# Performance work log

Measured on AMD Instinct MI355X. Metric: run time of the kernel, lower is better.

Reference implementation:

```python
import jax, jax.numpy as jnp
import numpy as np

N = 32768
F0, F1, F2, F3 = 16, 32, 64, 128
D0, D1, D2, D3 = (128, 128, 128), (64, 64, 64), (32, 32, 32), (16, 16, 16)
DST1, DST2, DTF = (16, 16, 16, 64), (64, 64, 32, 16), (4, 4, 4, 65536)
FST1, FST2, FTF = 64, 8, 8
TOTAL = 7 * (F0 + F1 + F2 + F3) + 9 * FST1 + 9 * FST2 + FTF  # 2336
INNER = 64
FACE3 = np.array([[1,0,0],[-1,0,0],[0,1,0],[0,-1,0],[0,0,1],[0,0,-1]], np.int32)
ST8 = np.concatenate([np.concatenate([FACE3, np.zeros((6,1), np.int32)], 1),
                      np.array([[0,0,0,1],[0,0,0,-1]], np.int32)], 0)

def rmsnorm(x, scale, eps=1e-8):
    rms = jnp.sqrt(jnp.mean(x * x, axis=-1, keepdims=True))
    return scale * x / (rms + eps)

def geglu(x):
    a, g = jnp.split(x, 2, axis=-1)
    return a * jax.nn.gelu(g)

def table_feats(table, p, offsets):
    # p in [0,1)^D -> scaled integer indices; gather base + modulo-wrapped neighbors
    dims = np.array(table.shape[:-1], np.int32)
    idx = (p * (dims - 1)).astype(jnp.int32)  # [N, D]
    base = table[tuple(idx[:, i] for i in range(idx.shape[-1]))]  # [N, F]
    if offsets is None:
        return base
    nbr = (idx[:, None, :] + offsets[None]) % dims  # [N, K, D]
    nf = table[tuple(nbr[..., i] for i in range(nbr.shape[-1]))]  # [N, K, F]
    return jnp.concatenate([base, nf.reshape(nf.shape[0], -1)], axis=-1)

def setup_inputs():
    key = jax.random.key(0)
    ks = jax.random.split(key, 20)
    tbl = lambda k, dims, f: jax.random.normal(k, dims + (f,), jnp.float32) * 0.1
    lin = lambda k, i, o: jax.random.normal(k, (i, o), jnp.float32) / np.sqrt(i).astype(np.float32)
    return dict(
        pos=jax.random.normal(ks[0], (N, 3), jnp.float32),
        dir=jax.random.normal(ks[1], (N, 3), jnp.float32),
        t=jax.random.uniform(ks[2], (N,), jnp.float32),
        table0=tbl(ks[3], D0, F0), table1=tbl(ks[4], D1, F1),
        table2=tbl(ks[5], D2, F2), table3=tbl(ks[6], D3, F3),
        st1=tbl(ks[7], DST1, FST1), st2=tbl(ks[8], DST2, FST2), tf=tbl(ks[9], DTF, FTF),
        sph_proj=lin(ks[10], 3, 8), tb1=jnp.zeros((1,), jnp.float32), tb2=jnp.zeros((1,), jnp.float32),
        gn1=jnp.ones((12,), jnp.float32), gw1=lin(ks[11], 12, 32),
        gn2=jnp.ones((16,), jnp.float32), gw2=lin(ks[12], 16, 32),
        gn3=jnp.ones((16,), jnp.float32), gw3=lin(ks[13], 16, 3),
        vn1=jnp.ones((TOTAL,), jnp.float32), vw1=lin(ks[14], TOTAL, 2 * TOTAL),
        vn2=jnp.ones((TOTAL,), jnp.float32), vw2=lin(ks[15], TOTAL, INNER),
        fw=lin(ks[16], INNER + 4, 4), fb=jnp.zeros((4,), jnp.float32))

def _forward(pos, dir, t, table0, table1, table2, table3, st1, st2, tf,
             sph_proj, tb1, tb2, gn1, gw1, gn2, gw2, gn3, gw3,
             vn1, vw1, vn2, vw2, fw, fb):
    # SphericalEmbedding
    rho = jnp.sqrt(jnp.sum(pos * pos, axis=-1, keepdims=True))
    phi = jnp.arctan2(pos[:, 1], pos[:, 0])
    theta = jnp.arccos(jnp.clip(pos[:, 2] / rho[:, 0], -1.0, 1.0))
    sph = jnp.stack([rho[:, 0], phi, theta], axis=-1) @ sph_proj  # [N, 8]
    # TimeEmbedding
    ct = jnp.cos(t[:, None] + tb1)
    st_ = jnp.sin(t[:, None] + tb2)
    temb = jnp.concatenate([ct, st_, jax.nn.silu(ct), jax.nn.silu(st_)], axis=-1)  # [N, 4]
    # geometric projection MLP -> normalized lookup coords
    h = jnp.concatenate([sph, temb], axis=-1)  # [N, 12]
    h = geglu(rmsnorm(h, gn1) @ gw1)  # [N, 16]
    h = geglu(rmsnorm(h, gn2) @ gw2)  # [N, 16]
    p = jax.nn.sigmoid(rmsnorm(h, gn3) @ gw3)  # [N, 3] in (0,1)
    pt = jnp.concatenate([p, t[:, None]], axis=-1)  # [N, 4]
    # multi-resolution gathers: base + 6 face neighbors per spatial table
    allf = jnp.concatenate([
        table_feats(table0, p, FACE3), table_feats(table1, p, FACE3),
        table_feats(table2, p, FACE3), table_feats(table3, p, FACE3),
        table_feats(st1, pt, ST8), table_feats(st2, pt, ST8),
        table_feats(tf, pt, None)], axis=-1)  # [N, TOTAL]
    # value MLP
    v = geglu(rmsnorm(allf, vn1) @ vw1)  # [N, TOTAL]
    down = rmsnorm(v, vn2) @ vw2  # [N, INNER]
    final_in = jnp.concatenate([down, p, t[:, None]], axis=-1)  # [N, INNER+4]
    return final_in @ fw + fb  # [N, 4]

def reference(pos, dir, t, table0, table1, table2, table3, st1, st2, tf,
              sph_proj, tb1, tb2, gn1, gw1, gn2, gw2, gn3, gw3,
              vn1, vw1, vn2, vw2, fw, fb):
    return _forward(pos, dir, t, table0, table1, table2, table3, st1, st2, tf,
                    sph_proj, tb1, tb2, gn1, gw1, gn2, gw2, gn3, gw3,
                    vn1, vw1, vn2, vw2, fw, fb)
```

## Files before the change

kernel.cpp:

```cpp
#include <hip/hip_runtime.h>
#include <hip/hip_bf16.h>
#include <stdint.h>

typedef __hip_bfloat16 bf16;
typedef __attribute__((ext_vector_type(8))) short v8s;
typedef __attribute__((ext_vector_type(4))) float v4f;

#define NPTS 32768
#define KTOT 2336
#define MPH2 2432
#define NBX2 19

#define AS1C(p) ((const __attribute__((address_space(1))) void*)(p))
#define AS3(p)  ((__attribute__((address_space(3))) void*)(p))

__device__ __forceinline__ float sigm(float x){ return 1.0f/(1.0f + expf(-x)); }
__device__ __forceinline__ float gelu_tanh(float x){
  float u = 0.7978845608028654f*(x + 0.044715f*x*x*x);
  return 0.5f*x*(1.0f + tanhf(u));
}
__device__ __forceinline__ float gelu_fast(float x){
  float u = 1.5957691216057308f*x*(1.0f + 0.044715f*x*x);
  return x / (1.0f + __expf(-u));
}

__global__ __launch_bounds__(256) void k_preamble(
    const float* __restrict__ pos, const float* __restrict__ t,
    const float* __restrict__ sph_proj, const float* __restrict__ tb1,
    const float* __restrict__ tb2,
    const float* __restrict__ gn1, const float* __restrict__ gw1,
    const float* __restrict__ gn2, const float* __restrict__ gw2,
    const float* __restrict__ gn3, const float* __restrict__ gw3,
    float4* __restrict__ Pbuf)
{
  int i = blockIdx.x*256 + threadIdx.x;
  if(i >= NPTS) return;
  float px = pos[3*i], py = pos[3*i+1], pz = pos[3*i+2];
  float rho = sqrtf(px*px + py*py + pz*pz);
  float phi = atan2f(py, px);
  float cz = fminf(1.0f, fmaxf(-1.0f, pz/rho));
  float theta = acosf(cz);
  float tv = t[i];
  float h[12];
  #pragma unroll
  for(int j=0;j<8;j++)
    h[j] = rho*sph_proj[j] + phi*sph_proj[8+j] + theta*sph_proj[16+j];
  float ct = cosf(tv + tb1[0]);
  float st = sinf(tv + tb2[0]);
  h[8]=ct; h[9]=st; h[10]=ct*sigm(ct); h[11]=st*sigm(st);

  float ss = 0.f;
  #pragma unroll
  for(int j=0;j<12;j++) ss += h[j]*h[j];
  float den = sqrtf(ss/12.0f) + 1e-8f;
  float hn[12];
  #pragma unroll
  for(int j=0;j<12;j++) hn[j] = gn1[j]*h[j]/den;

  float h2[16];
  #pragma unroll
  for(int j=0;j<16;j++){
    float a=0.f, g=0.f;
    #pragma unroll
    for(int k=0;k<12;k++){ a += hn[k]*gw1[k*32+j]; g += hn[k]*gw1[k*32+16+j]; }
    h2[j] = a*gelu_tanh(g);
  }
  ss = 0.f;
  #pragma unroll
  for(int j=0;j<16;j++) ss += h2[j]*h2[j];
  den = sqrtf(ss/16.0f) + 1e-8f;
  float hn2[16];
  #pragma unroll
  for(int j=0;j<16;j++) hn2[j] = gn2[j]*h2[j]/den;

  float h3[16];
  #pragma unroll
  for(int j=0;j<16;j++){
    float a=0.f, g=0.f;
    #pragma unroll
    for(int k=0;k<16;k++){ a += hn2[k]*gw2[k*32+j]; g += hn2[k]*gw2[k*32+16+j]; }
    h3[j] = a*gelu_tanh(g);
  }
  ss = 0.f;
  #pragma unroll
  for(int j=0;j<16;j++) ss += h3[j]*h3[j];
  den = sqrtf(ss/16.0f) + 1e-8f;
  float q[3];
  #pragma unroll
  for(int j=0;j<3;j++){
    float a=0.f;
    #pragma unroll
    for(int k=0;k<16;k++) a += (gn3[k]*h3[k]/den)*gw3[k*3+j];
    q[j] = sigm(a);
  }
  Pbuf[i] = make_float4(q[0], q[1], q[2], tv);
}

template<int F, int R>
__device__ __forceinline__ float rows_copyT(const float* __restrict__ T,
    const int (&offs)[R], bf16* __restrict__ dst, int lane){
  float ss = 0.f;
  if constexpr (F >= 64){
    #pragma unroll
    for(int r=0;r<R;r++){
      #pragma unroll
      for(int f0=0; f0<F; f0+=64){
        float v = T[(size_t)offs[r] + f0 + lane];
        dst[r*F + f0 + lane] = __float2bfloat16(v);
        ss += v*v;
      }
    }
  } else {
    constexpr int RPP = 64/F;
    int sub = lane / F;
    int f   = lane & (F-1);
    #pragma unroll
    for(int r0=0;r0<R;r0+=RPP){
      int r = r0 + sub;
      if(r < R){
        float v = T[(size_t)offs[r] + f];
        dst[r*F + f] = __float2bfloat16(v);
        ss += v*v;
      }
    }
  }
  return ss;
}

template<int F>
__device__ __forceinline__ float table3_gather(const float* __restrict__ T, int d,
    float p0, float p1, float p2, bf16* __restrict__ dst, int lane){
  int ix = (int)(p0*(float)(d-1));
  int iy = (int)(p1*(float)(d-1));
  int iz = (int)(p2*(float)(d-1));
  int xp = (ix+1>=d)?0:ix+1, xm = (ix==0)?d-1:ix-1;
  int yp = (iy+1>=d)?0:iy+1, ym = (iy==0)?d-1:iy-1;
  int zp = (iz+1>=d)?0:iz+1, zm = (iz==0)?d-1:iz-1;
  int offs[7] = {
    ((ix*d+iy)*d+iz)*F, ((xp*d+iy)*d+iz)*F, ((xm*d+iy)*d+iz)*F,
    ((ix*d+yp)*d+iz)*F, ((ix*d+ym)*d+iz)*F,
    ((ix*d+iy)*d+zp)*F, ((ix*d+iy)*d+zm)*F };
  return rows_copyT<F,7>(T, offs, dst, lane);
}

template<int F>
__device__ __forceinline__ float table4_gather(const float* __restrict__ T,
    int d0,int d1,int d2,int d3,
    float p0,float p1,float p2,float p3, bf16* __restrict__ dst, int lane){
  int ix = (int)(p0*(float)(d0-1));
  int iy = (int)(p1*(float)(d1-1));
  int iz = (int)(p2*(float)(d2-1));
  int iw = (int)(p3*(float)(d3-1));
  int xp=(ix+1>=d0)?0:ix+1, xm=(ix==0)?d0-1:ix-1;
  int yp=(iy+1>=d1)?0:iy+1, ym=(iy==0)?d1-1:iy-1;
  int zp=(iz+1>=d2)?0:iz+1, zm=(iz==0)?d2-1:iz-1;
  int wp=(iw+1>=d3)?0:iw+1, wm=(iw==0)?d3-1:iw-1;
  #define RO(x,y,z,w) (((((x)*d1 + (y))*d2 + (z))*d3 + (w))*F)
  int offs[9] = {
    RO(ix,iy,iz,iw), RO(xp,iy,iz,iw), RO(xm,iy,iz,iw),
    RO(ix,yp,iz,iw), RO(ix,ym,iz,iw), RO(ix,iy,zp,iw), RO(ix,iy,zm,iw),
    RO(ix,iy,iz,wp), RO(ix,iy,iz,wm) };
  #undef RO
  return rows_copyT<F,9>(T, offs, dst, lane);
}

__global__ __launch_bounds__(256) void k_gather(
    const float4* __restrict__ Pbuf,
    const float* __restrict__ T0, const float* __restrict__ T1,
    const float* __restrict__ T2, const float* __restrict__ T3,
    const float* __restrict__ S1, const float* __restrict__ S2,
    const float* __restrict__ TF,
    bf16* __restrict__ X, float* __restrict__ sx)
{
  int wave = threadIdx.x>>6, lane = threadIdx.x&63;
  int ptid = blockIdx.x*4 + wave;
  float4 P = Pbuf[ptid];
  bf16* dst = X + (size_t)ptid*KTOT;
  float ss = 0.f;
  ss += table3_gather<16 >(T0, 128, P.x, P.y, P.z, dst + 0,    lane);
  ss += table3_gather<32 >(T1,  64, P.x, P.y, P.z, dst + 112,  lane);
  ss += table3_gather<64 >(T2,  32, P.x, P.y, P.z, dst + 336,  lane);
  ss += table3_gather<128>(T3,  16, P.x, P.y, P.z, dst + 784,  lane);
  ss += table4_gather<64>(S1, 16,16,16,64, P.x,P.y,P.z,P.w, dst + 1680, lane);
  ss += table4_gather<8 >(S2, 64,64,32,16, P.x,P.y,P.z,P.w, dst + 2256, lane);
  {
    int ix=(int)(P.x*3.0f), iy=(int)(P.y*3.0f), iz=(int)(P.z*3.0f);
    int iw=(int)(P.w*65535.0f);
    int offs[1] = { (int)((((ix*4+iy)*4+iz))*65536 + iw)*8 };
    ss += rows_copyT<8,1>(TF, offs, dst + 2328, lane);
  }
  #pragma unroll
  for(int o=32;o>0;o>>=1) ss += __shfl_xor(ss, o);
  if(lane==0) sx[ptid] = 1.0f/(sqrtf(ss/2336.0f) + 1e-8f);
}

#define W1B_U4 ((2*MPH2*KTOT*2)/16)
__global__ __launch_bounds__(256) void k_w1zero(uint4* __restrict__ W1b){
  size_t idx = (size_t)blockIdx.x*256 + threadIdx.x;
  if(idx < (size_t)W1B_U4)
    W1b[idx] = make_uint4(0u,0u,0u,0u);
}

__global__ __launch_bounds__(256) void k_w1prep(const float* __restrict__ vw1,
                                                const float* __restrict__ vn1,
                                                bf16* __restrict__ W1b)
{
  __shared__ float tile[32][33];
  int h  = blockIdx.z;
  int m0 = blockIdx.x*32, k0 = blockIdx.y*32;
  int tx = threadIdx.x & 31, ty = threadIdx.x >> 5;
  #pragma unroll
  for(int dy=0; dy<32; dy+=8){
    int k = k0 + ty + dy;
    tile[ty+dy][tx] = vw1[(size_t)k*4672 + h*2336 + m0 + tx] * vn1[k];
  }
  __syncthreads();
  #pragma unroll
  for(int dy=0; dy<32; dy+=8){
    int m = m0 + ty + dy;
    W1b[(size_t)(h*MPH2 + m)*KTOT + k0 + tx] = __float2bfloat16(tile[tx][ty+dy]);
  }
}

__global__ __launch_bounds__(256) void k_w2prep(const float* __restrict__ vw2,
                                                const float* __restrict__ vn2,
                                                const float* __restrict__ fw,
                                                float4* __restrict__ W2f)
{
  int k = blockIdx.x*256 + threadIdx.x;
  if(k >= KTOT) return;
  float a0=0,a1=0,a2=0,a3=0;
  for(int i=0;i<64;i++){
    float w = vw2[k*64+i];
    a0 += w*fw[i*4+0]; a1 += w*fw[i*4+1]; a2 += w*fw[i*4+2]; a3 += w*fw[i*4+3];
  }
  float s = vn2[k];
  W2f[k] = make_float4(s*a0, s*a1, s*a2, s*a3);
}


#define PIPE_WAIT(NSTR) do{                                   \
    __builtin_amdgcn_sched_barrier(0);                        \
    asm volatile("s_waitcnt vmcnt(" NSTR ")" ::: "memory");   \
    __builtin_amdgcn_s_barrier();                             \
  }while(0)

template<int SB>
__device__ __forceinline__ void stage4(const bf16* aSrc, const bf16* bSrc, int k0e,
    bf16 (&As)[4][8192], bf16 (&Bs)[4][8192], int wave)
{
  __builtin_amdgcn_global_load_lds(AS1C(aSrc + k0e),            AS3(&As[SB][wave*512]),        16, 0, 0);
  __builtin_amdgcn_global_load_lds(AS1C(aSrc + 128*KTOT + k0e), AS3(&As[SB][4096 + wave*512]), 16, 0, 0);
  __builtin_amdgcn_global_load_lds(AS1C(bSrc + k0e),            AS3(&Bs[SB][wave*512]),        16, 0, 0);
  __builtin_amdgcn_global_load_lds(AS1C(bSrc + 64*KTOT + k0e),  AS3(&Bs[SB][4096 + wave*512]), 16, 0, 0);
}

template<int RB, int SB, bool STG>
__device__ __forceinline__ void body(const bf16* aSrc, const bf16* bSrc, int k0e,
    bf16 (&As)[4][8192], bf16 (&Bs)[4][8192], int wave, int aOff, int bOff,
    v4f (&acc)[8][4])
{
  v8s af[8]; v8s bb[4];
  #pragma unroll
  for(int i=0;i<8;i++) af[i] = *(const v8s*)(&As[RB][aOff + i*512]);
  #pragma unroll
  for(int j=0;j<4;j++) bb[j] = *(const v8s*)(&Bs[RB][bOff + j*512]);
  if constexpr (STG) stage4<SB>(aSrc, bSrc, k0e, As, Bs, wave);
  #pragma unroll
  for(int i=0;i<8;i++)
    #pragma unroll
    for(int j=0;j<4;j++)
      acc[i][j] = __builtin_amdgcn_mfma_f32_16x16x32_bf16(af[i], bb[j], acc[i][j], 0,0,0);
}

__global__ __launch_bounds__(512, 2) void k_gemm1(
    const bf16* __restrict__ X, const bf16* __restrict__ W1b,
    const float* __restrict__ sx, const float4* __restrict__ W2f,
    float* __restrict__ Part)
{
  __shared__ bf16 As[4][8192];
  __shared__ bf16 Bs[4][8192];
  int tid = threadIdx.x;
  int wave = tid>>6, lane = tid&63;

  int lid = blockIdx.x + 19*blockIdx.y;
  int swz = (lid & 7)*304 + (lid >> 3);
  int bx = swz % 19;
  int by = swz / 19;
  int row0 = by*256;
  int colh = bx*128;

  int wm = wave>>2, wn = wave&3;
  int lm = lane&15, lq = lane>>4;

  v4f acc[8][4];
  #pragma unroll
  for(int i=0;i<8;i++)
    #pragma unroll
    for(int j=0;j<4;j++)
      acc[i][j] = (v4f){0.f,0.f,0.f,0.f};

  int r0 = tid>>2;
  int qa = (tid&3) ^ ((tid>>3)&3);
  const bf16* aSrc = X + (size_t)(row0 + r0)*KTOT + qa*8;
  const bf16* bSrc = W1b + (size_t)(((r0>>5)&1)*MPH2 + colh + (r0>>6)*32 + (r0&31))*KTOT + qa*8;

  int swz4 = lq ^ ((lm>>1)&3);
  int aOff = ((wm*128 + lm)*4 + swz4)*8;
  int bOff = ((wn*64  + lm)*4 + swz4)*8;

  stage4<0>(aSrc, bSrc, 0,  As, Bs, wave);
  stage4<1>(aSrc, bSrc, 32, As, Bs, wave);
  stage4<2>(aSrc, bSrc, 64, As, Bs, wave);
  PIPE_WAIT("8");

  for(int t=0; t<68; t+=4){
    int ke = (t+3)*32;
    body<0,3,true>(aSrc,bSrc,ke,    As,Bs,wave,aOff,bOff,acc); PIPE_WAIT("8");
    body<1,0,true>(aSrc,bSrc,ke+32, As,Bs,wave,aOff,bOff,acc); PIPE_WAIT("8");
    body<2,1,true>(aSrc,bSrc,ke+64, As,Bs,wave,aOff,bOff,acc); PIPE_WAIT("8");
    body<3,2,true>(aSrc,bSrc,ke+96, As,Bs,wave,aOff,bOff,acc); PIPE_WAIT("8");
  }
  body<0,3,true >(aSrc,bSrc,71*32, As,Bs,wave,aOff,bOff,acc); PIPE_WAIT("8");
  body<1,0,true >(aSrc,bSrc,72*32, As,Bs,wave,aOff,bOff,acc); PIPE_WAIT("8");
  body<2,0,false>(aSrc,bSrc,0,     As,Bs,wave,aOff,bOff,acc); PIPE_WAIT("4");
  body<3,0,false>(aSrc,bSrc,0,     As,Bs,wave,aOff,bOff,acc); PIPE_WAIT("0");
  body<0,0,false>(aSrc,bSrc,0,     As,Bs,wave,aOff,bOff,acc);
  __syncthreads();

  float* red = (float*)&As[0][0];
  #pragma unroll
  for(int ph=0; ph<4; ph++){
    if(wn == ph){
      #pragma unroll
      for(int i=0;i<8;i++){
        #pragma unroll
        for(int r=0;r<4;r++){
          int lrow = wm*128 + i*16 + lq*4 + r;
          float s = sx[row0 + lrow];
          float d0=0,d1=0,d2=0,d3=0,ssq=0;
          #pragma unroll
          for(int j=0;j<2;j++){
            int c = colh + wn*32 + j*16 + lm;
            float va = s*acc[i][j][r];
            float vg = s*acc[i][j+2][r];
            float v  = va * gelu_fast(vg);
            int ci = c < KTOT ? c : KTOT-1;
            float4 w = W2f[ci];
            d0 += v*w.x; d1 += v*w.y; d2 += v*w.z; d3 += v*w.w;
            ssq += v*v;
          }
          #pragma unroll
          for(int o=1;o<16;o<<=1){
            d0 += __shfl_xor(d0,o); d1 += __shfl_xor(d1,o);
            d2 += __shfl_xor(d2,o); d3 += __shfl_xor(d3,o);
            ssq += __shfl_xor(ssq,o);
          }
          if(lm==0){
            if(ph==0){
              red[lrow*8+0]=d0; red[lrow*8+1]=d1; red[lrow*8+2]=d2;
              red[lrow*8+3]=d3; red[lrow*8+4]=ssq;
              red[lrow*8+5]=0.f; red[lrow*8+6]=0.f; red[lrow*8+7]=0.f;
            } else {
              red[lrow*8+0]+=d0; red[lrow*8+1]+=d1; red[lrow*8+2]+=d2;
              red[lrow*8+3]+=d3; red[lrow*8+4]+=ssq;
            }
          }
        }
      }
    }
    __syncthreads();
  }
  {
    int rr = tid >> 1, c4 = (tid & 1)*4;
    float4 val = *(float4*)&red[rr*8 + c4];
    *(float4*)&Part[((size_t)bx*NPTS + row0 + rr)*8 + c4] = val;
  }
}

__global__ __launch_bounds__(256) void k_finalize(const float* __restrict__ Part,
    const float4* __restrict__ Pbuf, const float* __restrict__ fw,
    const float* __restrict__ fb, float4* __restrict__ out)
{
  int row = blockIdx.x*256 + threadIdx.x;
  const float4* P4 = (const float4*)Part;
  float d0=0,d1=0,d2=0,d3=0,ss=0;
  for(int bx=0; bx<NBX2; bx++){
    size_t base = ((size_t)bx*NPTS + row)*2;
    float4 a = P4[base];
    float4 b = P4[base+1];
    d0+=a.x; d1+=a.y; d2+=a.z; d3+=a.w; ss+=b.x;
  }
  float sv = 1.0f/(sqrtf(ss/2336.0f)+1e-8f);
  float4 P = Pbuf[row];
  float o0 = sv*d0 + P.x*fw[256+0] + P.y*fw[260+0] + P.z*fw[264+0] + P.w*fw[268+0] + fb[0];
  float o1 = sv*d1 + P.x*fw[256+1] + P.y*fw[260+1] + P.z*fw[264+1] + P.w*fw[268+1] + fb[1];
  float o2 = sv*d2 + P.x*fw[256+2] + P.y*fw[260+2] + P.z*fw[264+2] + P.w*fw[268+2] + fb[2];
  float o3 = sv*d3 + P.x*fw[256+3] + P.y*fw[260+3] + P.z*fw[264+3] + P.w*fw[268+3] + fb[3];
  out[row] = make_float4(o0,o1,o2,o3);
}

extern "C" void kernel_launch(void* const* d_in, const int* in_sizes, int n_in,
                              void* d_out, int out_size, void* d_ws, size_t ws_size,
                              hipStream_t stream)
{
  const float* pos = (const float*)d_in[0];
  const float* t   = (const float*)d_in[2];
  const float* T0  = (const float*)d_in[3];
  const float* T1  = (const float*)d_in[4];
  const float* T2  = (const float*)d_in[5];
  const float* T3  = (const float*)d_in[6];
  const float* S1  = (const float*)d_in[7];
  const float* S2  = (const float*)d_in[8];
  const float* TF  = (const float*)d_in[9];
  const float* sph = (const float*)d_in[10];
  const float* tb1 = (const float*)d_in[11];
  const float* tb2 = (const float*)d_in[12];
  const float* gn1 = (const float*)d_in[13];
  const float* gw1 = (const float*)d_in[14];
  const float* gn2 = (const float*)d_in[15];
  const float* gw2 = (const float*)d_in[16];
  const float* gn3 = (const float*)d_in[17];
  const float* gw3 = (const float*)d_in[18];
  const float* vn1 = (const float*)d_in[19];
  const float* vw1 = (const float*)d_in[20];
  const float* vn2 = (const float*)d_in[21];
  const float* vw2 = (const float*)d_in[22];
  const float* fw  = (const float*)d_in[23];
  const float* fb  = (const float*)d_in[24];

  uint8_t* ws = (uint8_t*)d_ws;
  size_t off = 0;
  auto carve = [&](size_t bytes)->void*{
    void* pp = ws + off; off += (bytes + 255) & ~(size_t)255; return pp;
  };
  float4* Pbuf = (float4*)carve((size_t)NPTS*sizeof(float4));
  float*  sx   = (float*) carve((size_t)NPTS*sizeof(float));
  float4* W2f  = (float4*)carve((size_t)KTOT*sizeof(float4));
  bf16*   W1b  = (bf16*)  carve((size_t)2*MPH2*KTOT*sizeof(bf16));
  bf16*   X    = (bf16*)  carve((size_t)NPTS*KTOT*sizeof(bf16));
  float*  Part = (float*) carve((size_t)NBX2*NPTS*8*sizeof(float));

  k_preamble<<<NPTS/256, 256, 0, stream>>>(pos, t, sph, tb1, tb2,
                                           gn1, gw1, gn2, gw2, gn3, gw3, Pbuf);
  k_w1zero<<<(W1B_U4 + 255)/256, 256, 0, stream>>>((uint4*)W1b);
  k_w1prep<<<dim3(73,73,2), 256, 0, stream>>>(vw1, vn1, W1b);
  k_w2prep<<<(KTOT + 255)/256, 256, 0, stream>>>(vw2, vn2, fw, W2f);
  k_gather<<<NPTS/4, 256, 0, stream>>>(Pbuf, T0, T1, T2, T3, S1, S2, TF, X, sx);
  k_gemm1<<<dim3(19,128), 512, 0, stream>>>(X, W1b, sx, W2f, Part);
  k_finalize<<<NPTS/256, 256, 0, stream>>>(Part, Pbuf, fw, fb, (float4*)d_out);
}
```

Measured before the change: 1.614 ms.

## Split GEMM k-step into two phases with interleaved staging and setprio

Each k-step of the main GEMM now runs in two halves: the first loads half the A fragments plus B, issues the A prefetch, and runs 16 MFMAs. The second loads the other A half, issues the B prefetch, waits on vmcnt, and runs the remaining MFMAs. Extra workgroup barriers and s_setprio raises around the MFMA blocks are meant to keep waves in step and give matrix math priority over memory issue. This trades more barriers per k-step for finer-grained overlap of LDS reads, global-to-LDS staging and MFMA work.

Result: no change. 1.641 ms (+1.6%).

```diff
diff --git a/kernel.cpp b/kernel.cpp
--- a/kernel.cpp
+++ b/kernel.cpp
@@ -239,38 +239,66 @@
 }
 
 
-#define PIPE_WAIT(NSTR) do{                                   \
-    __builtin_amdgcn_sched_barrier(0);                        \
-    asm volatile("s_waitcnt vmcnt(" NSTR ")" ::: "memory");   \
-    __builtin_amdgcn_s_barrier();                             \
-  }while(0)
+template<int W> __device__ __forceinline__ void vwait(){
+  if constexpr (W==8)      asm volatile("s_waitcnt vmcnt(8)" ::: "memory");
+  else if constexpr (W==4) asm volatile("s_waitcnt vmcnt(4)" ::: "memory");
+  else                     asm volatile("s_waitcnt vmcnt(0)" ::: "memory");
+}
 
 template<int SB>
-__device__ __forceinline__ void stage4(const bf16* aSrc, const bf16* bSrc, int k0e,
-    bf16 (&As)[4][8192], bf16 (&Bs)[4][8192], int wave)
-{
+__device__ __forceinline__ void stageA2(const bf16* aSrc, int k0e,
+    bf16 (&As)[4][8192], int wave){
   __builtin_amdgcn_global_load_lds(AS1C(aSrc + k0e),            AS3(&As[SB][wave*512]),        16, 0, 0);
   __builtin_amdgcn_global_load_lds(AS1C(aSrc + 128*KTOT + k0e), AS3(&As[SB][4096 + wave*512]), 16, 0, 0);
+}
+template<int SB>
+__device__ __forceinline__ void stageB2(const bf16* bSrc, int k0e,
+    bf16 (&Bs)[4][8192], int wave){
   __builtin_amdgcn_global_load_lds(AS1C(bSrc + k0e),            AS3(&Bs[SB][wave*512]),        16, 0, 0);
   __builtin_amdgcn_global_load_lds(AS1C(bSrc + 64*KTOT + k0e),  AS3(&Bs[SB][4096 + wave*512]), 16, 0, 0);
 }
 
-template<int RB, int SB, bool STG>
-__device__ __forceinline__ void body(const bf16* aSrc, const bf16* bSrc, int k0e,
+template<int RB, int SB, bool STG, int W>
+__device__ __forceinline__ void tile2ph(const bf16* aSrc, const bf16* bSrc, int ke,
     bf16 (&As)[4][8192], bf16 (&Bs)[4][8192], int wave, int aOff, int bOff,
     v4f (&acc)[8][4])
 {
-  v8s af[8]; v8s bb[4];
-  #pragma unroll
-  for(int i=0;i<8;i++) af[i] = *(const v8s*)(&As[RB][aOff + i*512]);
-  #pragma unroll
-  for(int j=0;j<4;j++) bb[j] = *(const v8s*)(&Bs[RB][bOff + j*512]);
-  if constexpr (STG) stage4<SB>(aSrc, bSrc, k0e, As, Bs, wave);
-  #pragma unroll
-  for(int i=0;i<8;i++)
+  v8s af0[4], bb[4], af1[4];
+  #pragma unroll
+  for(int i=0;i<4;i++) af0[i] = *(const v8s*)(&As[RB][aOff + i*512]);
+  #pragma unroll
+  for(int j=0;j<4;j++) bb[j]  = *(const v8s*)(&Bs[RB][bOff + j*512]);
+  if constexpr (STG) stageA2<SB>(aSrc, ke, As, wave);
+  __builtin_amdgcn_sched_barrier(0);
+  __builtin_amdgcn_s_barrier();
+  __builtin_amdgcn_sched_barrier(0);
+  __builtin_amdgcn_s_setprio(1);
+  #pragma unroll
+  for(int i=0;i<4;i++)
     #pragma unroll
     for(int j=0;j<4;j++)
-      acc[i][j] = __builtin_amdgcn_mfma_f32_16x16x32_bf16(af[i], bb[j], acc[i][j], 0,0,0);
+      acc[i][j] = __builtin_amdgcn_mfma_f32_16x16x32_bf16(af0[i], bb[j], acc[i][j], 0,0,0);
+  __builtin_amdgcn_s_setprio(0);
+  __builtin_amdgcn_sched_barrier(0);
+  __builtin_amdgcn_s_barrier();
+  __builtin_amdgcn_sched_barrier(0);
+  #pragma unroll
+  for(int i=0;i<4;i++) af1[i] = *(const v8s*)(&As[RB][aOff + (i+4)*512]);
+  if constexpr (STG) stageB2<SB>(bSrc, ke, Bs, wave);
+  __builtin_amdgcn_sched_barrier(0);
+  vwait<W>();
+  __builtin_amdgcn_s_barrier();
+  __builtin_amdgcn_sched_barrier(0);
+  __builtin_amdgcn_s_setprio(1);
+  #pragma unroll
+  for(int i=0;i<4;i++)
+    #pragma unroll
+    for(int j=0;j<4;j++)
+      acc[i+4][j] = __builtin_amdgcn_mfma_f32_16x16x32_bf16(af1[i], bb[j], acc[i+4][j], 0,0,0);
+  __builtin_amdgcn_s_setprio(0);
+  __builtin_amdgcn_sched_barrier(0);
+  __builtin_amdgcn_s_barrier();
+  __builtin_amdgcn_sched_barrier(0);
 }
 
 __global__ __launch_bounds__(512, 2) void k_gemm1(
@@ -309,23 +337,26 @@
   int aOff = ((wm*128 + lm)*4 + swz4)*8;
   int bOff = ((wn*64  + lm)*4 + swz4)*8;
 
-  stage4<0>(aSrc, bSrc, 0,  As, Bs, wave);
-  stage4<1>(aSrc, bSrc, 32, As, Bs, wave);
-  stage4<2>(aSrc, bSrc, 64, As, Bs, wave);
-  PIPE_WAIT("8");
+  stageA2<0>(aSrc, 0,  As, wave); stageB2<0>(bSrc, 0,  Bs, wave);
+  stageA2<1>(aSrc, 32, As, wave); stageB2<1>(bSrc, 32, Bs, wave);
+  stageA2<2>(aSrc, 64, As, wave); stageB2<2>(bSrc, 64, Bs, wave);
+  __builtin_amdgcn_sched_barrier(0);
+  vwait<8>();
+  __builtin_amdgcn_s_barrier();
+  __builtin_amdgcn_sched_barrier(0);
 
   for(int t=0; t<68; t+=4){
     int ke = (t+3)*32;
-    body<0,3,true>(aSrc,bSrc,ke,    As,Bs,wave,aOff,bOff,acc); PIPE_WAIT("8");
-    body<1,0,true>(aSrc,bSrc,ke+32, As,Bs,wave,aOff,bOff,acc); PIPE_WAIT("8");
-    body<2,1,true>(aSrc,bSrc,ke+64, As,Bs,wave,aOff,bOff,acc); PIPE_WAIT("8");
-    body<3,2,true>(aSrc,bSrc,ke+96, As,Bs,wave,aOff,bOff,acc); PIPE_WAIT("8");
-  }
-  body<0,3,true >(aSrc,bSrc,71*32, As,Bs,wave,aOff,bOff,acc); PIPE_WAIT("8");
-  body<1,0,true >(aSrc,bSrc,72*32, As,Bs,wave,aOff,bOff,acc); PIPE_WAIT("8");
-  body<2,0,false>(aSrc,bSrc,0,     As,Bs,wave,aOff,bOff,acc); PIPE_WAIT("4");
-  body<3,0,false>(aSrc,bSrc,0,     As,Bs,wave,aOff,bOff,acc); PIPE_WAIT("0");
-  body<0,0,false>(aSrc,bSrc,0,     As,Bs,wave,aOff,bOff,acc);
+    tile2ph<0,3,true,8>(aSrc,bSrc,ke,    As,Bs,wave,aOff,bOff,acc);
+    tile2ph<1,0,true,8>(aSrc,bSrc,ke+32, As,Bs,wave,aOff,bOff,acc);
+    tile2ph<2,1,true,8>(aSrc,bSrc,ke+64, As,Bs,wave,aOff,bOff,acc);
+    tile2ph<3,2,true,8>(aSrc,bSrc,ke+96, As,Bs,wave,aOff,bOff,acc);
+  }
+  tile2ph<0,3,true ,8>(aSrc,bSrc,71*32, As,Bs,wave,aOff,bOff,acc);
+  tile2ph<1,0,true ,8>(aSrc,bSrc,72*32, As,Bs,wave,aOff,bOff,acc);
+  tile2ph<2,1,false,4>(aSrc,bSrc,0,     As,Bs,wave,aOff,bOff,acc);
+  tile2ph<3,2,false,0>(aSrc,bSrc,0,     As,Bs,wave,aOff,bOff,acc);
+  tile2ph<0,3,false,0>(aSrc,bSrc,0,     As,Bs,wave,aOff,bOff,acc);
   __syncthreads();
 
   float* red = (float*)&As[0][0];
```
